# Kernel tuning notes

Hardware: AMD Instinct MI355X
Metric: run time of the kernel (lower is better)

## Reference

```python
import jax, jax.numpy as jnp
import numpy as np

N_NODES = 100000
N_EDGES = 1600000
N_GRAPHS = 1024
IN_G, HID_G = 64, 128
IN_T, H1, H2 = 200, 256, 128
CONCAT = 2 * HID_G + H2  # 384


def setup_inputs() -> dict:
    key = jax.random.key(0)
    ks = jax.random.split(key, 24)
    def lin(k, fin, fout):
        kw, kb = jax.random.split(k)
        s = 1.0 / np.sqrt(fin)
        return (jax.random.uniform(kw, (fin, fout), jnp.float32, -s, s),
                jax.random.uniform(kb, (fout,), jnp.float32, -s, s))
    Wg1, bg1 = lin(ks[0], IN_G, HID_G)
    Wg2, bg2 = lin(ks[1], HID_G, HID_G)
    Wg3, bg3 = lin(ks[2], HID_G, HID_G)
    Wg4, bg4 = lin(ks[3], HID_G, HID_G)
    Wt1, bt1 = lin(ks[4], IN_T, H1)
    Wt2, bt2 = lin(ks[5], H1, H2)
    Wf1, bf1 = lin(ks[6], CONCAT, H1)
    Wf2, bf2 = lin(ks[7], H1, H2)
    Wf3, bf3 = lin(ks[8], H2, 1)
    x_graph = jax.random.normal(ks[9], (N_NODES, IN_G), jnp.float32)
    edge_index = jax.random.randint(ks[10], (2, N_EDGES), 0, N_NODES, jnp.int32)
    batch = jnp.sort(jax.random.randint(ks[11], (N_NODES,), 0, N_GRAPHS, jnp.int32))
    x_tabular = jax.random.normal(ks[12], (N_GRAPHS, IN_T), jnp.float32)
    return {"x_graph": x_graph, "edge_index": edge_index, "batch": batch,
            "x_tabular": x_tabular,
            "Wg1": Wg1, "bg1": bg1, "Wg2": Wg2, "bg2": bg2,
            "Wg3": Wg3, "bg3": bg3, "Wg4": Wg4, "bg4": bg4,
            "Wt1": Wt1, "bt1": bt1, "Wt2": Wt2, "bt2": bt2,
            "Wf1": Wf1, "bf1": bf1, "Wf2": Wf2, "bf2": bf2,
            "Wf3": Wf3, "bf3": bf3}


def _gcn(x, src, dst, norm, W, b, n):
    # x' = D^-1/2 A_hat D^-1/2 (x W) + b, scatter-add over edges
    h = x @ W
    msg = h[src] * norm[:, None]
    return jax.ops.segment_sum(msg, dst, num_segments=n) + b


def reference(x_graph, edge_index, batch, x_tabular,
              Wg1, bg1, Wg2, bg2, Wg3, bg3, Wg4, bg4,
              Wt1, bt1, Wt2, bt2, Wf1, bf1, Wf2, bf2, Wf3, bf3):
    n = x_graph.shape[0]
    b = x_tabular.shape[0]
    ar = jnp.arange(n, dtype=edge_index.dtype)
    # self-loops added once in Multi_Modal.forward + once inside GCNConv (default)
    src = jnp.concatenate([edge_index[0], ar, ar])
    dst = jnp.concatenate([edge_index[1], ar, ar])
    deg = jax.ops.segment_sum(jnp.ones(src.shape, x_graph.dtype), dst, num_segments=n)
    dinv = jnp.where(deg > 0, jax.lax.rsqrt(deg), 0.0)
    norm = dinv[src] * dinv[dst]
    h = jax.nn.relu(_gcn(x_graph, src, dst, norm, Wg1, bg1, n))
    h = jax.nn.relu(_gcn(h, src, dst, norm, Wg2, bg2, n))
    h = jax.nn.relu(_gcn(h, src, dst, norm, Wg3, bg3, n))
    h = jax.nn.relu(_gcn(h, src, dst, norm, Wg4, bg4, n))
    # global mean/max pool per graph
    cnt = jax.ops.segment_sum(jnp.ones((n,), h.dtype), batch, num_segments=b)
    mean = jax.ops.segment_sum(h, batch, num_segments=b) / jnp.maximum(cnt, 1.0)[:, None]
    mx = jax.ops.segment_max(h, batch, num_segments=b)
    x1 = jnp.concatenate([mean, mx], axis=1)
    # tabular branch
    x2 = jax.nn.relu(jax.nn.relu(x_tabular @ Wt1 + bt1) @ Wt2 + bt2)
    # fused head
    x = jnp.concatenate([x1, x2], axis=1)
    x = jax.nn.relu(x @ Wf1 + bf1)
    x = jax.nn.relu(x @ Wf2 + bf2)
    return jax.nn.sigmoid(x @ Wf3 + bf3)
```

## Files before the change

kernel.cpp:

```cpp
#include <hip/hip_runtime.h>
#include <hip/hip_bf16.h>
#include <math.h>

#define N_NODES  100000
#define N_EDGES  1600000
#define N_GRAPHS 1024

typedef __hip_bfloat16 bf16;
typedef unsigned short u16;
typedef unsigned int   u32;
typedef __attribute__((ext_vector_type(8))) short bf8_t;
typedef __attribute__((ext_vector_type(4))) float f4_t;

__device__ __forceinline__ float b2f(bf16 v) { return __bfloat162float(v); }
__device__ __forceinline__ u16 bfbits(float f) {
    bf16 h = __float2bfloat16(f);
    return *reinterpret_cast<u16*>(&h);
}
__device__ __forceinline__ float lo_bf(u32 u) { return __uint_as_float(u << 16); }
__device__ __forceinline__ float hi_bf(u32 u) { return __uint_as_float(u & 0xffff0000u); }

__global__ void sniff_dtype(const u16* __restrict__ p, int* __restrict__ flag) {
    if (blockIdx.x == 0 && threadIdx.x == 0) {
        int bad = 0;
        for (int i = 0; i < 256; ++i) {
            float f = __uint_as_float(((u32)p[i]) << 16);
            if (!(fabsf(f) < 100.f)) bad++;
        }
        *flag = (bad == 0) ? 1 : 0;
    }
}

#define NT 18
struct WTask { const void* src; void* dst; int n; int mode; int K; };
struct PrepArgs { WTask t[NT]; int bstart[NT]; };

__global__ void prep_k(PrepArgs args, const int* __restrict__ flag) {
    int b = blockIdx.x, ti = 0;
    while (ti < NT - 1 && b >= args.bstart[ti + 1]) ++ti;
    int idx = (b - args.bstart[ti]) * 256 + threadIdx.x;
    WTask tk = args.t[ti];
    if (idx >= tk.n) return;
    int isb = *flag;
    if (tk.mode == 0) {
        float v = isb ? b2f(((const bf16*)tk.src)[idx]) : ((const float*)tk.src)[idx];
        ((float*)tk.dst)[idx] = v;
    } else {
        int bseg = idx >> 9, r = idx & 511;
        int L = r >> 3, j = r & 7;
        int kb = bseg >> 3, tt = bseg & 7;
        int k = kb * 32 + ((L >> 4) << 3) + j;
        int n = (tt << 4) + (L & 15);
        int so = k * 128 + n;
        float v = isb ? b2f(((const bf16*)tk.src)[so]) : ((const float*)tk.src)[so];
        ((u16*)tk.dst)[idx] = bfbits(v);
    }
}

__global__ void cvt_b(const void* __restrict__ src, u16* __restrict__ dst,
                      int n, const int* __restrict__ flag) {
    int i = blockIdx.x * blockDim.x + threadIdx.x;
    if (i >= n) return;
    if (*flag) dst[i] = ((const u16*)src)[i];
    else       dst[i] = bfbits(((const float*)src)[i]);
}

__global__ void deg_init(int* degi) {
    int i = blockIdx.x * blockDim.x + threadIdx.x;
    if (i < N_NODES) degi[i] = 2;
}

__global__ void deg_edges(const int* __restrict__ dst, int* __restrict__ degi) {
    int e = blockIdx.x * blockDim.x + threadIdx.x;
    if (e < N_EDGES) atomicAdd(&degi[dst[e]], 1);
}

__global__ void dinv_k(const int* __restrict__ degi, float* __restrict__ dinv) {
    int i = blockIdx.x * blockDim.x + threadIdx.x;
    if (i < N_NODES) dinv[i] = rsqrtf((float)degi[i]);
}

#define SCAN_B 256
__global__ void scan1(const int* __restrict__ degi, int* __restrict__ ex,
                      int* __restrict__ bsum) {
    __shared__ int s[SCAN_B];
    int i = blockIdx.x * SCAN_B + threadIdx.x;
    int v = (i < N_NODES) ? (degi[i] - 2) : 0;
    s[threadIdx.x] = v;
    __syncthreads();
    for (int off = 1; off < SCAN_B; off <<= 1) {
        int t = (threadIdx.x >= off) ? s[threadIdx.x - off] : 0;
        __syncthreads();
        if (threadIdx.x >= off) s[threadIdx.x] += t;
        __syncthreads();
    }
    if (i < N_NODES) ex[i] = s[threadIdx.x] - v;
    if (threadIdx.x == SCAN_B - 1) bsum[blockIdx.x] = s[SCAN_B - 1];
}

__global__ void scan2(int* __restrict__ bsum, int nb) {
    __shared__ int s[512];
    int i = threadIdx.x;
    int v = (i < nb) ? bsum[i] : 0;
    s[i] = v;
    __syncthreads();
    for (int off = 1; off < 512; off <<= 1) {
        int t = (i >= off) ? s[i - off] : 0;
        __syncthreads();
        if (i >= off) s[i] += t;
        __syncthreads();
    }
    if (i < nb) bsum[i] = s[i] - v;
}

__global__ void scan3(int* __restrict__ rowptr, const int* __restrict__ bsum,
                      int* __restrict__ cnt) {
    int i = blockIdx.x * SCAN_B + threadIdx.x;
    if (i >= N_NODES) return;
    rowptr[i] += bsum[blockIdx.x];
    cnt[i] = 0;
}

__global__ void fill_csr(const int* __restrict__ src, const int* __restrict__ dst,
                         const float* __restrict__ dinv, const int* __restrict__ rowptr,
                         int* __restrict__ cnt, int2* __restrict__ csrp) {
    int e = blockIdx.x * 256 + threadIdx.x;
    if (e >= N_EDGES) return;
    int s = src[e], d = dst[e];
    int pos = rowptr[d] + atomicAdd(&cnt[d], 1);
    csrp[pos] = make_int2(s, __float_as_int(dinv[s] * dinv[d]));
}

template<int K, bool EPI>
__global__ __launch_bounds__(256) void gemm_mfma(const u16* __restrict__ A,
        const u16* __restrict__ Wm, const float* __restrict__ bias,
        u16* __restrict__ Out, int M)
{
    int wave = threadIdx.x >> 6, lane = threadIdx.x & 63;
    int rowBase = blockIdx.x * 64 + wave * 16;
    int quad = lane >> 4, low = lane & 15;
    int arow = rowBase + low;
    if (arow >= M) arow = M - 1;
    const u16* ap = A + (size_t)arow * K + quad * 8;

    f4_t acc[8];
#pragma unroll
    for (int t = 0; t < 8; ++t) acc[t] = (f4_t)(0.f);

#pragma unroll
    for (int kb = 0; kb < K / 32; ++kb) {
        bf8_t a = *(const bf8_t*)(ap + kb * 32);
#pragma unroll
        for (int t = 0; t < 8; ++t) {
            bf8_t b = *(const bf8_t*)(Wm + (((kb << 3) + t) << 9) + lane * 8);
            acc[t] = __builtin_amdgcn_mfma_f32_16x16x32_bf16(a, b, acc[t], 0, 0, 0);
        }
    }

    int orow0 = rowBase + quad * 4;
#pragma unroll
    for (int t = 0; t < 8; ++t) {
        float bn = EPI ? bias[t * 16 + low] : 0.f;
#pragma unroll
        for (int j = 0; j < 4; ++j) {
            int r = orow0 + j;
            float v = acc[t][j];
            if (EPI) v = fmaxf(v + bn, 0.f);
            if (r < M) Out[(size_t)r * 128 + t * 16 + low] = bfbits(v);
        }
    }
}

__global__ __launch_bounds__(256) void gather_x(
        const int* __restrict__ rowptr, const int* __restrict__ cnt,
        const int2* __restrict__ csrp, const u16* __restrict__ X,
        const float* __restrict__ dinv, u16* __restrict__ G)
{
    int node = blockIdx.x * 4 + (threadIdx.x >> 6);
    if (node >= N_NODES) return;
    int lane = threadIdx.x & 63;
    int half = lane >> 5, fi = lane & 31;
    const u32* X2 = (const u32*)X;
    float accx = 0.f, accy = 0.f;
    if (half == 0) {
        float dv = dinv[node];
        float s = 2.f * dv * dv;
        u32 h0 = X2[(size_t)node * 32 + fi];
        accx = s * lo_bf(h0); accy = s * hi_bf(h0);
    }
    int rp = rowptr[node];
    int end = rp + cnt[node];
    int p = rp + half;
    for (; p + 8 <= end; p += 8) {
        int2 m0 = csrp[p],     m1 = csrp[p + 2];
        int2 m2 = csrp[p + 4], m3 = csrp[p + 6];
        u32 v0 = X2[(size_t)m0.x * 32 + fi];
        u32 v1 = X2[(size_t)m1.x * 32 + fi];
        u32 v2 = X2[(size_t)m2.x * 32 + fi];
        u32 v3 = X2[(size_t)m3.x * 32 + fi];
        float w0 = __int_as_float(m0.y), w1 = __int_as_float(m1.y);
        float w2 = __int_as_float(m2.y), w3 = __int_as_float(m3.y);
        accx += w0 * lo_bf(v0) + w1 * lo_bf(v1) + w2 * lo_bf(v2) + w3 * lo_bf(v3);
        accy += w0 * hi_bf(v0) + w1 * hi_bf(v1) + w2 * hi_bf(v2) + w3 * hi_bf(v3);
    }
    for (; p < end; p += 2) {
        int2 m = csrp[p];
        u32 v = X2[(size_t)m.x * 32 + fi];
        float w = __int_as_float(m.y);
        accx += w * lo_bf(v); accy += w * hi_bf(v);
    }
    accx += __shfl_xor(accx, 32);
    accy += __shfl_xor(accy, 32);
    if (half == 0) {
        u32 pack = ((u32)bfbits(accy) << 16) | (u32)bfbits(accx);
        ((u32*)G)[(size_t)node * 32 + fi] = pack;
    }
}

__global__ __launch_bounds__(256) void gather_agg(
        const int* __restrict__ rowptr, const int* __restrict__ cnt,
        const int2* __restrict__ csrp, const u16* __restrict__ H,
        const float* __restrict__ dinv, const float* __restrict__ bias,
        u16* __restrict__ A)
{
    int node = blockIdx.x * 4 + (threadIdx.x >> 6);
    if (node >= N_NODES) return;
    int lane = threadIdx.x & 63;
    const u32* H2 = (const u32*)H;
    float2 bb = ((const float2*)bias)[lane];
    float dv = dinv[node];
    float selfw = 2.f * dv * dv;
    u32 h0 = H2[(size_t)node * 64 + lane];
    float accx = bb.x + selfw * lo_bf(h0);
    float accy = bb.y + selfw * hi_bf(h0);
    int p = rowptr[node];
    int end = p + cnt[node];
    for (; p + 8 <= end; p += 8) {
        int2 m0 = csrp[p],     m1 = csrp[p + 1];
        int2 m2 = csrp[p + 2], m3 = csrp[p + 3];
        int2 m4 = csrp[p + 4], m5 = csrp[p + 5];
        int2 m6 = csrp[p + 6], m7 = csrp[p + 7];
        u32 v0 = H2[(size_t)m0.x * 64 + lane];
        u32 v1 = H2[(size_t)m1.x * 64 + lane];
        u32 v2 = H2[(size_t)m2.x * 64 + lane];
        u32 v3 = H2[(size_t)m3.x * 64 + lane];
        u32 v4 = H2[(size_t)m4.x * 64 + lane];
        u32 v5 = H2[(size_t)m5.x * 64 + lane];
        u32 v6 = H2[(size_t)m6.x * 64 + lane];
        u32 v7 = H2[(size_t)m7.x * 64 + lane];
        float w0 = __int_as_float(m0.y), w1 = __int_as_float(m1.y);
        float w2 = __int_as_float(m2.y), w3 = __int_as_float(m3.y);
        float w4 = __int_as_float(m4.y), w5 = __int_as_float(m5.y);
        float w6 = __int_as_float(m6.y), w7 = __int_as_float(m7.y);
        accx += w0 * lo_bf(v0) + w1 * lo_bf(v1) + w2 * lo_bf(v2) + w3 * lo_bf(v3)
              + w4 * lo_bf(v4) + w5 * lo_bf(v5) + w6 * lo_bf(v6) + w7 * lo_bf(v7);
        accy += w0 * hi_bf(v0) + w1 * hi_bf(v1) + w2 * hi_bf(v2) + w3 * hi_bf(v3)
              + w4 * hi_bf(v4) + w5 * hi_bf(v5) + w6 * hi_bf(v6) + w7 * hi_bf(v7);
    }
    for (; p < end; ++p) {
        int2 m = csrp[p];
        u32 v = H2[(size_t)m.x * 64 + lane];
        float w = __int_as_float(m.y);
        accx += w * lo_bf(v); accy += w * hi_bf(v);
    }
    accx = fmaxf(accx, 0.f);
    accy = fmaxf(accy, 0.f);
    u32 pack = ((u32)bfbits(accy) << 16) | (u32)bfbits(accx);
    ((u32*)A)[(size_t)node * 64 + lane] = pack;
}

__global__ __launch_bounds__(128) void pool_k(const u16* __restrict__ A,
        const int* __restrict__ batch, float* __restrict__ concat)
{
    __shared__ int sb[2];
    int g = blockIdx.x;
    if (threadIdx.x == 0) {
        int lo = 0, hi = N_NODES;
        while (lo < hi) { int m = (lo + hi) >> 1; if (batch[m] < g) lo = m + 1; else hi = m; }
        sb[0] = lo;
        hi = N_NODES;
        while (lo < hi) { int m = (lo + hi) >> 1; if (batch[m] < g + 1) lo = m + 1; else hi = m; }
        sb[1] = lo;
    }
    __syncthreads();
    int start = sb[0], end = sb[1];
    int t = threadIdx.x;
    float sum = 0.f, mx = -3.4e38f;
    for (int n = start; n < end; ++n) {
        float v = __uint_as_float(((u32)A[(size_t)n * 128 + t]) << 16);
        sum += v; mx = fmaxf(mx, v);
    }
    int cnt = end - start;
    float mean = sum / (float)(cnt > 0 ? cnt : 1);
    if (cnt == 0) mx = 0.f;
    concat[g * 384 + t] = mean;
    concat[g * 384 + 128 + t] = mx;
}

template<int KD, bool EXT>
__global__ void rowmm(const void* __restrict__ Xv, int ldx,
                      const float* __restrict__ W, const float* __restrict__ bias,
                      float* __restrict__ out, int ldo, const int* __restrict__ flagp)
{
    extern __shared__ float xs[];
    int g = blockIdx.x;
    int col = threadIdx.x;
    int N = blockDim.x;
    const int isb = EXT ? *flagp : 0;
    for (int k = col; k < KD; k += N) {
        size_t off = (size_t)g * ldx + k;
        xs[k] = EXT ? (isb ? b2f(((const bf16*)Xv)[off]) : ((const float*)Xv)[off])
                    : ((const float*)Xv)[off];
    }
    __syncthreads();
    float acc = bias[col];
    for (int k = 0; k < KD; ++k)
        acc += xs[k] * W[(size_t)k * N + col];
    out[(size_t)g * ldo + col] = fmaxf(acc, 0.f);
}

__global__ __launch_bounds__(256) void head3(const float* __restrict__ u2,
        const float* __restrict__ Wf3, const float* __restrict__ bf3,
        void* __restrict__ out, const int* __restrict__ flagp)
{
    int g = blockIdx.x * 4 + (threadIdx.x >> 6);
    int lane = threadIdx.x & 63;
    float2 v = ((const float2*)(u2 + (size_t)g * 128))[lane];
    float2 w = ((const float2*)Wf3)[lane];
    float acc = v.x * w.x + v.y * w.y;
    for (int off = 32; off > 0; off >>= 1) acc += __shfl_down(acc, off);
    if (lane == 0) {
        float z = acc + bf3[0];
        float sg = 1.f / (1.f + expf(-z));
        if (*flagp) ((bf16*)out)[g] = __float2bfloat16(sg);
        else        ((float*)out)[g] = sg;
    }
}

extern "C" void kernel_launch(void* const* d_in, const int* in_sizes, int n_in,
                              void* d_out, int out_size, void* d_ws, size_t ws_size,
                              hipStream_t stream) {
    const void* x_graph    = d_in[0];
    const int*  edge_index = (const int*)d_in[1];
    const int*  batch      = (const int*)d_in[2];
    const void* x_tab      = d_in[3];

    const int* src  = edge_index;
    const int* dstp = edge_index + N_EDGES;

    char* wsp = (char*)d_ws;
    int*  flag = (int*)wsp;                      wsp += 16;
    u16*  A16  = (u16*)wsp;                      wsp += (size_t)N_NODES * 128 * 2;
    u16*  B16  = (u16*)wsp;                      wsp += (size_t)N_NODES * 128 * 2;
    u16*  X16  = (u16*)wsp;                      wsp += (size_t)N_NODES * 64 * 2;
    u16*  G16  = (u16*)wsp;                      wsp += (size_t)N_NODES * 64 * 2;
    u16*  Wm[4];
    Wm[0] = (u16*)wsp;                           wsp += 64 * 128 * 2;
    Wm[1] = (u16*)wsp;                           wsp += 128 * 128 * 2;
    Wm[2] = (u16*)wsp;                           wsp += 128 * 128 * 2;
    Wm[3] = (u16*)wsp;                           wsp += 128 * 128 * 2;
    float* p = (float*)wsp;
    float* bg1f = p; p += 128;
    float* bg2f = p; p += 128;
    float* bg3f = p; p += 128;
    float* bg4f = p; p += 128;
    float* Wt1f = p; p += 200 * 256; float* bt1f = p; p += 256;
    float* Wt2f = p; p += 256 * 128; float* bt2f = p; p += 128;
    float* Wf1f = p; p += 384 * 256; float* bf1f = p; p += 256;
    float* Wf2f = p; p += 256 * 128; float* bf2f = p; p += 128;
    float* Wf3f = p; p += 128;       float* bf3f = p; p += 4;
    int*   degi   = (int*)p;            p += N_NODES;
    float* dinv   = p;                  p += N_NODES;
    int*   rowptr = (int*)p;            p += N_NODES;
    int*   cnt    = (int*)p;            p += N_NODES;
    int*   bsum   = (int*)p;            p += 512;
    int2*  csrp   = (int2*)p;           p += 2 * N_EDGES;
    float* concat = p;                  p += N_GRAPHS * 384;
    float* t1     = p;                  p += N_GRAPHS * 256;
    float* u1     = p;                  p += N_GRAPHS * 256;
    float* u2     = p;                  p += N_GRAPHS * 128;

    sniff_dtype<<<1, 64, 0, stream>>>((const u16*)x_graph, flag);

    PrepArgs pa;
    auto setT = [&](int i, const void* s, void* d, int n, int mode, int K) {
        pa.t[i].src = s; pa.t[i].dst = d; pa.t[i].n = n; pa.t[i].mode = mode; pa.t[i].K = K;
    };
    setT(0,  d_in[4],  Wm[0], 64 * 128, 1, 64);
    setT(1,  d_in[6],  Wm[1], 128 * 128, 1, 128);
    setT(2,  d_in[8],  Wm[2], 128 * 128, 1, 128);
    setT(3,  d_in[10], Wm[3], 128 * 128, 1, 128);
    setT(4,  d_in[12], Wt1f, 200 * 256, 0, 0);
    setT(5,  d_in[14], Wt2f, 256 * 128, 0, 0);
    setT(6,  d_in[16], Wf1f, 384 * 256, 0, 0);
    setT(7,  d_in[18], Wf2f, 256 * 128, 0, 0);
    setT(8,  d_in[20], Wf3f, 128, 0, 0);
    setT(9,  d_in[5],  bg1f, 128, 0, 0);
    setT(10, d_in[7],  bg2f, 128, 0, 0);
    setT(11, d_in[9],  bg3f, 128, 0, 0);
    setT(12, d_in[11], bg4f, 128, 0, 0);
    setT(13, d_in[13], bt1f, 256, 0, 0);
    setT(14, d_in[15], bt2f, 128, 0, 0);
    setT(15, d_in[17], bf1f, 256, 0, 0);
    setT(16, d_in[19], bf2f, 128, 0, 0);
    setT(17, d_in[21], bf3f, 1, 0, 0);
    int totalBlocks = 0;
    for (int i = 0; i < NT; ++i) {
        pa.bstart[i] = totalBlocks;
        totalBlocks += (pa.t[i].n + 255) / 256;
    }
    prep_k<<<totalBlocks, 256, 0, stream>>>(pa, flag);
    cvt_b<<<(N_NODES * 64 + 255) / 256, 256, 0, stream>>>(x_graph, X16, N_NODES * 64, flag);

    const int nb = (N_NODES + SCAN_B - 1) / SCAN_B;
    deg_init<<<(N_NODES + 255) / 256, 256, 0, stream>>>(degi);
    deg_edges<<<(N_EDGES + 255) / 256, 256, 0, stream>>>(dstp, degi);
    dinv_k<<<(N_NODES + 255) / 256, 256, 0, stream>>>(degi, dinv);
    scan1<<<nb, SCAN_B, 0, stream>>>(degi, rowptr, bsum);
    scan2<<<1, 512, 0, stream>>>(bsum, nb);
    scan3<<<nb, SCAN_B, 0, stream>>>(rowptr, bsum, cnt);
    fill_csr<<<(N_EDGES + 255) / 256, 256, 0, stream>>>(src, dstp, dinv, rowptr, cnt, csrp);

    const int gemmGrid = (N_NODES + 63) / 64;
    const int aggGrid  = (N_NODES + 3) / 4;

    gather_x<<<aggGrid, 256, 0, stream>>>(rowptr, cnt, csrp, X16, dinv, G16);
    gemm_mfma<64, true><<<gemmGrid, 256, 0, stream>>>(G16, Wm[0], bg1f, A16, N_NODES);

    const float* bgL[4] = {bg1f, bg2f, bg3f, bg4f};
    for (int l = 1; l < 4; ++l) {
        gemm_mfma<128, false><<<gemmGrid, 256, 0, stream>>>(A16, Wm[l], nullptr, B16, N_NODES);
        gather_agg<<<aggGrid, 256, 0, stream>>>(rowptr, cnt, csrp, B16, dinv, bgL[l], A16);
    }

    pool_k<<<N_GRAPHS, 128, 0, stream>>>(A16, batch, concat);

    rowmm<200, true><<<N_GRAPHS, 256, 200 * 4, stream>>>(x_tab, 200, Wt1f, bt1f, t1, 256, flag);
    rowmm<256, false><<<N_GRAPHS, 128, 256 * 4, stream>>>(t1, 256, Wt2f, bt2f, concat + 256, 384, flag);

    rowmm<384, false><<<N_GRAPHS, 256, 384 * 4, stream>>>(concat, 384, Wf1f, bf1f, u1, 256, flag);
    rowmm<256, false><<<N_GRAPHS, 128, 256 * 4, stream>>>(u1, 256, Wf2f, bf2f, u2, 128, flag);
    head3<<<N_GRAPHS / 4, 256, 0, stream>>>(u2, Wf3f, bf3f, d_out, flag);
}
```

Before: 772.7 us.

## Use feature-chunked node layout and packed 4-byte CSR entries for gathers

Node feature matrices now use a chunk-major layout of 16-feature slices (32 bytes per node per chunk), and the gather kernels handle one chunk per block so each chunk's working set is smaller and more cache-friendly. CSR entries are packed into 32 bits: a 17-bit source index plus a 15-bit quantized dinv[src], with dinv[dst] applied once at the end. This halves edge-list traffic. The GEMM, conversion and pooling kernels are updated to read and write the new layout. The quantized edge weight loses precision, and the edge list is now re-read once per chunk, multiplying index traffic.

```diff
diff --git a/kernel.cpp b/kernel.cpp
--- a/kernel.cpp
+++ b/kernel.cpp
@@ -57,12 +57,15 @@
     }
 }
 
-__global__ void cvt_b(const void* __restrict__ src, u16* __restrict__ dst,
-                      int n, const int* __restrict__ flag) {
+__global__ void cvt_xc(const void* __restrict__ src, u16* __restrict__ dst,
+                       const int* __restrict__ flag) {
     int i = blockIdx.x * blockDim.x + threadIdx.x;
-    if (i >= n) return;
-    if (*flag) dst[i] = ((const u16*)src)[i];
-    else       dst[i] = bfbits(((const float*)src)[i]);
+    if (i >= N_NODES * 64) return;
+    int node = i >> 6, f = i & 63;
+    u16 v;
+    if (*flag) v = ((const u16*)src)[i];
+    else       v = bfbits(((const float*)src)[i]);
+    dst[((size_t)(f >> 4) * N_NODES + node) * 16 + (f & 15)] = v;
 }
 
 __global__ void deg_init(int* degi) {
@@ -123,12 +126,13 @@
 
 __global__ void fill_csr(const int* __restrict__ src, const int* __restrict__ dst,
                          const float* __restrict__ dinv, const int* __restrict__ rowptr,
-                         int* __restrict__ cnt, int2* __restrict__ csrp) {
+                         int* __restrict__ cnt, u32* __restrict__ csr4) {
     int e = blockIdx.x * 256 + threadIdx.x;
     if (e >= N_EDGES) return;
     int s = src[e], d = dst[e];
     int pos = rowptr[d] + atomicAdd(&cnt[d], 1);
-    csrp[pos] = make_int2(s, __float_as_int(dinv[s] * dinv[d]));
+    u32 q = (u32)__float2int_rn(dinv[s] * 32767.f);
+    csr4[pos] = (q << 17) | (u32)s;
 }
 
 template<int K, bool EPI>
@@ -141,7 +145,6 @@
     int quad = lane >> 4, low = lane & 15;
     int arow = rowBase + low;
     if (arow >= M) arow = M - 1;
-    const u16* ap = A + (size_t)arow * K + quad * 8;
 
     f4_t acc[8];
 #pragma unroll
@@ -149,7 +152,9 @@
 
 #pragma unroll
     for (int kb = 0; kb < K / 32; ++kb) {
-        bf8_t a = *(const bf8_t*)(ap + kb * 32);
+        const u16* ap = A + ((size_t)((kb << 1) + (quad >> 1)) * N_NODES + arow) * 16
+                          + ((quad & 1) << 3);
+        bf8_t a = *(const bf8_t*)ap;
 #pragma unroll
         for (int t = 0; t < 8; ++t) {
             bf8_t b = *(const bf8_t*)(Wm + (((kb << 3) + t) << 9) + lane * 8);
@@ -166,107 +171,55 @@
             int r = orow0 + j;
             float v = acc[t][j];
             if (EPI) v = fmaxf(v + bn, 0.f);
-            if (r < M) Out[(size_t)r * 128 + t * 16 + low] = bfbits(v);
+            if (r < M) Out[((size_t)t * N_NODES + r) * 16 + low] = bfbits(v);
         }
     }
 }
 
-__global__ __launch_bounds__(256) void gather_x(
+template<int CBITS, bool EPI>
+__global__ __launch_bounds__(512) void gather_c(
         const int* __restrict__ rowptr, const int* __restrict__ cnt,
-        const int2* __restrict__ csrp, const u16* __restrict__ X,
-        const float* __restrict__ dinv, u16* __restrict__ G)
-{
-    int node = blockIdx.x * 4 + (threadIdx.x >> 6);
+        const u32* __restrict__ csr4, const u16* __restrict__ Hc,
+        const float* __restrict__ dinv, const float* __restrict__ bias,
+        u16* __restrict__ Ac)
+{
+    const int NCH = 1 << CBITS;
+    int chunk = blockIdx.x & (NCH - 1);
+    int node = (blockIdx.x >> CBITS) * 8 + (threadIdx.x >> 6);
     if (node >= N_NODES) return;
     int lane = threadIdx.x & 63;
-    int half = lane >> 5, fi = lane & 31;
-    const u32* X2 = (const u32*)X;
+    int es = lane >> 3, fi = lane & 7;
+    const u32* Hrow = (const u32*)Hc + (size_t)chunk * N_NODES * 8;
+    float dv = dinv[node];
     float accx = 0.f, accy = 0.f;
-    if (half == 0) {
-        float dv = dinv[node];
-        float s = 2.f * dv * dv;
-        u32 h0 = X2[(size_t)node * 32 + fi];
-        accx = s * lo_bf(h0); accy = s * hi_bf(h0);
+    if (es == 0) {
+        u32 h = Hrow[(size_t)node * 8 + fi];
+        float w = 2.f * dv;
+        accx = w * lo_bf(h); accy = w * hi_bf(h);
     }
     int rp = rowptr[node];
     int end = rp + cnt[node];
-    int p = rp + half;
-    for (; p + 8 <= end; p += 8) {
-        int2 m0 = csrp[p],     m1 = csrp[p + 2];
-        int2 m2 = csrp[p + 4], m3 = csrp[p + 6];
-        u32 v0 = X2[(size_t)m0.x * 32 + fi];
-        u32 v1 = X2[(size_t)m1.x * 32 + fi];
-        u32 v2 = X2[(size_t)m2.x * 32 + fi];
-        u32 v3 = X2[(size_t)m3.x * 32 + fi];
-        float w0 = __int_as_float(m0.y), w1 = __int_as_float(m1.y);
-        float w2 = __int_as_float(m2.y), w3 = __int_as_float(m3.y);
-        accx += w0 * lo_bf(v0) + w1 * lo_bf(v1) + w2 * lo_bf(v2) + w3 * lo_bf(v3);
-        accy += w0 * hi_bf(v0) + w1 * hi_bf(v1) + w2 * hi_bf(v2) + w3 * hi_bf(v3);
-    }
-    for (; p < end; p += 2) {
-        int2 m = csrp[p];
-        u32 v = X2[(size_t)m.x * 32 + fi];
-        float w = __int_as_float(m.y);
-        accx += w * lo_bf(v); accy += w * hi_bf(v);
-    }
-    accx += __shfl_xor(accx, 32);
-    accy += __shfl_xor(accy, 32);
-    if (half == 0) {
+    for (int p = rp + es; p < end; p += 8) {
+        u32 m = csr4[p];
+        int s = (int)(m & 0x1FFFFu);
+        float w = (float)(m >> 17) * (1.f / 32767.f);
+        u32 h = Hrow[(size_t)s * 8 + fi];
+        accx += w * lo_bf(h);
+        accy += w * hi_bf(h);
+    }
+    accx += __shfl_xor(accx, 8);  accy += __shfl_xor(accy, 8);
+    accx += __shfl_xor(accx, 16); accy += __shfl_xor(accy, 16);
+    accx += __shfl_xor(accx, 32); accy += __shfl_xor(accy, 32);
+    if (es == 0) {
+        accx *= dv; accy *= dv;
+        if (EPI) {
+            float2 bb = ((const float2*)bias)[chunk * 8 + fi];
+            accx = fmaxf(accx + bb.x, 0.f);
+            accy = fmaxf(accy + bb.y, 0.f);
+        }
         u32 pack = ((u32)bfbits(accy) << 16) | (u32)bfbits(accx);
-        ((u32*)G)[(size_t)node * 32 + fi] = pack;
-    }
-}
-
-__global__ __launch_bounds__(256) void gather_agg(
-        const int* __restrict__ rowptr, const int* __restrict__ cnt,
-        const int2* __restrict__ csrp, const u16* __restrict__ H,
-        const float* __restrict__ dinv, const float* __restrict__ bias,
-        u16* __restrict__ A)
-{
-    int node = blockIdx.x * 4 + (threadIdx.x >> 6);
-    if (node >= N_NODES) return;
-    int lane = threadIdx.x & 63;
-    const u32* H2 = (const u32*)H;
-    float2 bb = ((const float2*)bias)[lane];
-    float dv = dinv[node];
-    float selfw = 2.f * dv * dv;
-    u32 h0 = H2[(size_t)node * 64 + lane];
-    float accx = bb.x + selfw * lo_bf(h0);
-    float accy = bb.y + selfw * hi_bf(h0);
-    int p = rowptr[node];
-    int end = p + cnt[node];
-    for (; p + 8 <= end; p += 8) {
-        int2 m0 = csrp[p],     m1 = csrp[p + 1];
-        int2 m2 = csrp[p + 2], m3 = csrp[p + 3];
-        int2 m4 = csrp[p + 4], m5 = csrp[p + 5];
-        int2 m6 = csrp[p + 6], m7 = csrp[p + 7];
-        u32 v0 = H2[(size_t)m0.x * 64 + lane];
-        u32 v1 = H2[(size_t)m1.x * 64 + lane];
-        u32 v2 = H2[(size_t)m2.x * 64 + lane];
-        u32 v3 = H2[(size_t)m3.x * 64 + lane];
-        u32 v4 = H2[(size_t)m4.x * 64 + lane];
-        u32 v5 = H2[(size_t)m5.x * 64 + lane];
-        u32 v6 = H2[(size_t)m6.x * 64 + lane];
-        u32 v7 = H2[(size_t)m7.x * 64 + lane];
-        float w0 = __int_as_float(m0.y), w1 = __int_as_float(m1.y);
-        float w2 = __int_as_float(m2.y), w3 = __int_as_float(m3.y);
-        float w4 = __int_as_float(m4.y), w5 = __int_as_float(m5.y);
-        float w6 = __int_as_float(m6.y), w7 = __int_as_float(m7.y);
-        accx += w0 * lo_bf(v0) + w1 * lo_bf(v1) + w2 * lo_bf(v2) + w3 * lo_bf(v3)
-              + w4 * lo_bf(v4) + w5 * lo_bf(v5) + w6 * lo_bf(v6) + w7 * lo_bf(v7);
-        accy += w0 * hi_bf(v0) + w1 * hi_bf(v1) + w2 * hi_bf(v2) + w3 * hi_bf(v3)
-              + w4 * hi_bf(v4) + w5 * hi_bf(v5) + w6 * hi_bf(v6) + w7 * hi_bf(v7);
-    }
-    for (; p < end; ++p) {
-        int2 m = csrp[p];
-        u32 v = H2[(size_t)m.x * 64 + lane];
-        float w = __int_as_float(m.y);
-        accx += w * lo_bf(v); accy += w * hi_bf(v);
-    }
-    accx = fmaxf(accx, 0.f);
-    accy = fmaxf(accy, 0.f);
-    u32 pack = ((u32)bfbits(accy) << 16) | (u32)bfbits(accx);
-    ((u32*)A)[(size_t)node * 64 + lane] = pack;
+        ((u32*)Ac)[((size_t)chunk * N_NODES + node) * 8 + fi] = pack;
+    }
 }
 
 __global__ __launch_bounds__(128) void pool_k(const u16* __restrict__ A,
@@ -285,9 +238,10 @@
     __syncthreads();
     int start = sb[0], end = sb[1];
     int t = threadIdx.x;
+    const u16* Ap = A + (size_t)(t >> 4) * N_NODES * 16 + (t & 15);
     float sum = 0.f, mx = -3.4e38f;
     for (int n = start; n < end; ++n) {
-        float v = __uint_as_float(((u32)A[(size_t)n * 128 + t]) << 16);
+        float v = __uint_as_float(((u32)Ap[(size_t)n * 16]) << 16);
         sum += v; mx = fmaxf(mx, v);
     }
     int cnt = end - start;
@@ -374,7 +328,7 @@
     int*   rowptr = (int*)p;            p += N_NODES;
     int*   cnt    = (int*)p;            p += N_NODES;
     int*   bsum   = (int*)p;            p += 512;
-    int2*  csrp   = (int2*)p;           p += 2 * N_EDGES;
+    u32*   csr4   = (u32*)p;            p += N_EDGES;
     float* concat = p;                  p += N_GRAPHS * 384;
     float* t1     = p;                  p += N_GRAPHS * 256;
     float* u1     = p;                  p += N_GRAPHS * 256;
@@ -410,7 +364,7 @@
         totalBlocks += (pa.t[i].n + 255) / 256;
     }
     prep_k<<<totalBlocks, 256, 0, stream>>>(pa, flag);
-    cvt_b<<<(N_NODES * 64 + 255) / 256, 256, 0, stream>>>(x_graph, X16, N_NODES * 64, flag);
+    cvt_xc<<<(N_NODES * 64 + 255) / 256, 256, 0, stream>>>(x_graph, X16, flag);
 
     const int nb = (N_NODES + SCAN_B - 1) / SCAN_B;
     deg_init<<<(N_NODES + 255) / 256, 256, 0, stream>>>(degi);
@@ -419,18 +373,19 @@
     scan1<<<nb, SCAN_B, 0, stream>>>(degi, rowptr, bsum);
     scan2<<<1, 512, 0, stream>>>(bsum, nb);
     scan3<<<nb, SCAN_B, 0, stream>>>(rowptr, bsum, cnt);
-    fill_csr<<<(N_EDGES + 255) / 256, 256, 0, stream>>>(src, dstp, dinv, rowptr, cnt, csrp);
+    fill_csr<<<(N_EDGES + 255) / 256, 256, 0, stream>>>(src, dstp, dinv, rowptr, cnt, csr4);
 
     const int gemmGrid = (N_NODES + 63) / 64;
-    const int aggGrid  = (N_NODES + 3) / 4;
-
-    gather_x<<<aggGrid, 256, 0, stream>>>(rowptr, cnt, csrp, X16, dinv, G16);
+    const int ggrid8   = ((N_NODES + 7) / 8) * 8;
+    const int ggrid4   = ((N_NODES + 7) / 8) * 4;
+
+    gather_c<2, false><<<ggrid4, 512, 0, stream>>>(rowptr, cnt, csr4, X16, dinv, nullptr, G16);
     gemm_mfma<64, true><<<gemmGrid, 256, 0, stream>>>(G16, Wm[0], bg1f, A16, N_NODES);
 
     const float* bgL[4] = {bg1f, bg2f, bg3f, bg4f};
     for (int l = 1; l < 4; ++l) {
         gemm_mfma<128, false><<<gemmGrid, 256, 0, stream>>>(A16, Wm[l], nullptr, B16, N_NODES);
-        gather_agg<<<aggGrid, 256, 0, stream>>>(rowptr, cnt, csrp, B16, dinv, bgL[l], A16);
+        gather_c<3, true><<<ggrid8, 512, 0, stream>>>(rowptr, cnt, csr4, B16, dinv, bgL[l], A16);
     }
 
     pool_k<<<N_GRAPHS, 128, 0, stream>>>(A16, batch, concat);
```

Result: slower. 1.354 ms (+75.3%).
